# Performance work log

Measured on AMD Instinct MI355X. Metric: run time of the kernel, lower is better.

Reference implementation:

```python
import jax, jax.numpy as jnp
import numpy as np

EPS = 1e-3  # keras LayerNormalization default epsilon

def layer_norm(x, gamma, beta):
    mu = jnp.mean(x, axis=-1, keepdims=True)
    var = jnp.var(x, axis=-1, keepdims=True)
    return (x - mu) * jax.lax.rsqrt(var + EPS) * gamma + beta

def setup_inputs() -> dict:
    key = jax.random.key(0)
    ks = jax.random.split(key, 10)
    B, N, FD, AD, PD, DP = 4, 512, 256, 256, 128, 64
    s = lambda k, *sh: jax.random.normal(k, sh, dtype=jnp.float32)
    return {
        "F": s(ks[0], B, N, FD),
        "D": s(ks[1], B, N, N, DP),
        "Wq": s(ks[2], FD, AD) / np.sqrt(FD),
        "Wk": s(ks[3], FD, AD) / np.sqrt(FD),
        "Wv": s(ks[4], FD, AD) / np.sqrt(FD),
        "g_f": jnp.ones((FD,), jnp.float32),
        "b_f": jnp.zeros((FD,), jnp.float32),
        "g_p": jnp.ones((DP,), jnp.float32),
        "b_p": jnp.zeros((DP,), jnp.float32),
        "W_pt": s(ks[5], DP, PD) / np.sqrt(DP),
        "b_pt": jnp.zeros((PD,), jnp.float32),
        "W_ph": s(ks[6], PD, 1) / np.sqrt(PD),
    }

def reference(F, D, Wq, Wk, Wv, g_f, b_f, g_p, b_p, W_pt, b_pt, W_ph):
    # features path
    Fn = layer_norm(F, g_f, b_f)                       # [B,N,FD]
    Q = Fn @ Wq                                        # [B,N,AD]
    K = Fn @ Wk
    V = Fn @ Wv
    # pair-bias path: LN -> Dense(pairs_dim)+bias -> Dense(num_heads=1)
    Bn = layer_norm(D, g_p, b_p)                       # [B,N,N,DP]
    Bt = Bn @ W_pt + b_pt                              # [B,N,N,PD]
    bias = (Bt @ W_ph)[..., 0]                         # [B,N,N]
    scalar = 1.0 / jnp.sqrt(jnp.float32(Q.shape[-1]))
    A = jnp.einsum('bqd,bkd->bqk', Q, K) + bias        # QK^T + pair bias
    A = jax.nn.softmax(scalar * A, axis=-1)
    O = jnp.einsum('bqk,bkd->bqd', A, V)               # [B,N,AD]
    return jnp.sum(O, axis=-1)                         # [B,N]
```

## Files before the change

kernel.cpp:

```cpp
#include <hip/hip_runtime.h>
#include <cstddef>
#include <cstdint>

#define OFF_GW    0
#define OFF_WV    64
#define OFF_SC    320
#define OFF_VSUM  384
#define OFF_Q     2432
#define OFF_KT    526720
#define OFF_BIAS  1051008

typedef float v4f __attribute__((ext_vector_type(4)));
typedef float v2f __attribute__((ext_vector_type(2)));

__global__ __launch_bounds__(256) void k0_consts(
    const float* __restrict__ Wv, const float* __restrict__ g_p,
    const float* __restrict__ b_p, const float* __restrict__ W_pt,
    const float* __restrict__ b_pt, const float* __restrict__ W_ph,
    float* __restrict__ ws) {
  int t = threadIdx.x;
  if (blockIdx.x < 64) {
    int row = blockIdx.x * 4 + (t >> 6);
    int l = t & 63;
    float s = 0.f;
#pragma unroll
    for (int j = 0; j < 4; ++j) s += Wv[row * 256 + l + 64 * j];
    for (int m = 32; m >= 1; m >>= 1) s += __shfl_xor(s, m);
    if (l == 0) ws[OFF_WV + row] = s;
  } else {
    __shared__ float wc_s[64];
    __shared__ float wph_s[128];
    if (t < 128) wph_s[t] = W_ph[t];
    __syncthreads();
    int c = t >> 2, sub = t & 3;
    float wc = 0.f;
#pragma unroll
    for (int j = 0; j < 32; ++j)
      wc += W_pt[c * 128 + sub * 32 + j] * wph_s[sub * 32 + j];
    wc += __shfl_xor(wc, 1);
    wc += __shfl_xor(wc, 2);
    if (sub == 0) {
      wc_s[c] = wc;
      ws[OFF_GW + c] = g_p[c] * wc;
    }
    __syncthreads();
    if (t == 0) {
      float sg = 0.f, bc = 0.f;
      for (int cc = 0; cc < 64; ++cc) {
        sg += g_p[cc] * wc_s[cc];
        bc += b_p[cc] * wc_s[cc];
      }
      for (int p = 0; p < 128; ++p) bc += b_pt[p] * wph_s[p];
      ws[OFF_SC] = sg;
      ws[OFF_SC + 1] = bc;
    }
  }
}

__global__ __launch_bounds__(256, 4) void kf_proj_bias(
    const float* __restrict__ F, const float* __restrict__ Wq,
    const float* __restrict__ Wk, const float* __restrict__ g_f,
    const float* __restrict__ b_f, const float* __restrict__ D,
    float* __restrict__ ws) {
  __shared__ __align__(16) float fn[8][260];
  __shared__ float smu[8], srn[8];
  __shared__ __align__(16) float gws[64];
  int t = threadIdx.x;

  if (blockIdx.x >= 512) {
    if (t < 64) gws[t] = ws[OFF_GW + t];
    float sum_gw = ws[OFF_SC];
    float bconst = ws[OFF_SC + 1];
    __syncthreads();

    int e = (blockIdx.x - 512) * 256 + t;
    const v4f* ep = (const v4f*)(D + (size_t)e * 64);
    v4f x[16];
#pragma unroll
    for (int p = 0; p < 16; ++p) x[p] = ep[p];
    float s1 = 0.f, s2 = 0.f, sw = 0.f;
#pragma unroll
    for (int p = 0; p < 16; ++p) {
      v4f xx = x[p];
      v4f gv = *(const v4f*)(&gws[p * 4]);
      s1 += xx.x + xx.y + xx.z + xx.w;
      s2 += xx.x * xx.x + xx.y * xx.y + xx.z * xx.z + xx.w * xx.w;
      sw += xx.x * gv.x + xx.y * gv.y + xx.z * gv.z + xx.w * gv.w;
    }
    float mu = s1 * (1.f / 64.f);
    float var = s2 * (1.f / 64.f) - mu * mu;
    float rn = rsqrtf(var + 1e-3f);
    ws[OFF_BIAS + e] = (rn * (sw - mu * sum_gw) + bconst) * 0.0625f;
    return;
  }

  int g = blockIdx.x >> 1, h = blockIdx.x & 1;
  int row0 = g * 8;
  const float* Fp = F + (size_t)row0 * 256;
#pragma unroll
  for (int k = 0; k < 8; ++k) fn[k][t] = Fp[k * 256 + t];
  __syncthreads();
  int r = t >> 5, l32 = t & 31;
  float s1 = 0.f, s2 = 0.f;
#pragma unroll
  for (int m = 0; m < 8; ++m) {
    float x = fn[r][l32 + 32 * m];
    s1 += x;
    s2 += x * x;
  }
  for (int m = 16; m >= 1; m >>= 1) {
    s1 += __shfl_xor(s1, m);
    s2 += __shfl_xor(s2, m);
  }
  if (l32 == 0) {
    float mu = s1 * (1.f / 256.f);
    float var = s2 * (1.f / 256.f) - mu * mu;
    smu[r] = mu;
    srn[r] = rsqrtf(var + 1e-3f);
  }
  __syncthreads();
  float gf = g_f[t], bf = b_f[t];
#pragma unroll
  for (int k = 0; k < 8; ++k)
    fn[k][t] = (fn[k][t] - smu[k]) * srn[k] * gf + bf;
  __syncthreads();
  if (h == 0) {
    const float* wv = ws + OFF_WV;
    float s = 0.f;
#pragma unroll
    for (int m = 0; m < 8; ++m) s += fn[r][l32 + 32 * m] * wv[l32 + 32 * m];
    for (int m = 16; m >= 1; m >>= 1) s += __shfl_xor(s, m);
    if (l32 == 0) ws[OFF_VSUM + row0 + r] = s;
  }
  int matsel = t >> 7;
  int col = h * 128 + (t & 127);
  const float* W = matsel ? Wk : Wq;
  float acc[8] = {0, 0, 0, 0, 0, 0, 0, 0};
#pragma unroll 2
  for (int f = 0; f < 256; f += 4) {
    float w0 = W[(f + 0) * 256 + col];
    float w1 = W[(f + 1) * 256 + col];
    float w2 = W[(f + 2) * 256 + col];
    float w3 = W[(f + 3) * 256 + col];
#pragma unroll
    for (int k = 0; k < 8; ++k) {
      v4f x = *(const v4f*)(&fn[k][f]);
      acc[k] = fmaf(x.w, w3,
               fmaf(x.z, w2, fmaf(x.y, w1, fmaf(x.x, w0, acc[k]))));
    }
  }
  if (matsel == 0) {
    float* Out = ws + OFF_Q + (size_t)row0 * 256 + col;
#pragma unroll
    for (int k = 0; k < 8; ++k) Out[k * 256] = acc[k];
  } else {
    int bb = row0 >> 9, r0b = row0 & 511;
    float* Out = ws + OFF_KT + (size_t)bb * 131072 + (size_t)col * 512 + r0b;
    v4f o0 = {acc[0], acc[1], acc[2], acc[3]};
    v4f o1 = {acc[4], acc[5], acc[6], acc[7]};
    *(v4f*)Out = o0;
    *(v4f*)(Out + 4) = o1;
  }
}

__global__ __launch_bounds__(256) void kb2_attn(
    const float* __restrict__ ws, float* __restrict__ out) {
  __shared__ float Sx[4][512];
  __shared__ __align__(16) float Qs[4][256];
  __shared__ float vs[512];
  int t = threadIdx.x;
  int w = t >> 6, l = t & 63;
  int b = blockIdx.x >> 7, tile = blockIdx.x & 127;
  int rowbase = b * 512 + tile * 4;

#pragma unroll
  for (int k = 0; k < 4; ++k)
    Qs[k][t] = ws[OFF_Q + (size_t)(rowbase + k) * 256 + t];
  vs[t] = ws[OFF_VSUM + b * 512 + t];
  vs[t + 256] = ws[OFF_VSUM + b * 512 + 256 + t];
  const float* bb = ws + OFF_BIAS + (size_t)rowbase * 512;
#pragma unroll
  for (int rr = 0; rr < 4; ++rr) {
    Sx[rr][t] = bb[rr * 512 + t];
    Sx[rr][t + 256] = bb[rr * 512 + 256 + t];
  }
  __syncthreads();

  const float* Ktb = ws + OFF_KT + (size_t)b * 131072;
  float a0[4] = {0, 0, 0, 0}, a1[4] = {0, 0, 0, 0};
#pragma unroll 2
  for (int f4 = 0; f4 < 64; ++f4) {
    v4f qv0 = *(const v4f*)(&Qs[0][f4 * 4]);
    v4f qv1 = *(const v4f*)(&Qs[1][f4 * 4]);
    v4f qv2 = *(const v4f*)(&Qs[2][f4 * 4]);
    v4f qv3 = *(const v4f*)(&Qs[3][f4 * 4]);
#pragma unroll
    for (int ff = 0; ff < 4; ++ff) {
      v2f kv = *(const v2f*)(Ktb + (size_t)(f4 * 4 + ff) * 512 + 2 * t);
      a0[0] += qv0[ff] * kv.x; a1[0] += qv0[ff] * kv.y;
      a0[1] += qv1[ff] * kv.x; a1[1] += qv1[ff] * kv.y;
      a0[2] += qv2[ff] * kv.x; a1[2] += qv2[ff] * kv.y;
      a0[3] += qv3[ff] * kv.x; a1[3] += qv3[ff] * kv.y;
    }
  }
#pragma unroll
  for (int rr = 0; rr < 4; ++rr) {
    Sx[rr][2 * t]     += a0[rr] * 0.0625f;
    Sx[rr][2 * t + 1] += a1[rr] * 0.0625f;
  }
  __syncthreads();

  float m = -1e30f;
#pragma unroll
  for (int j = 0; j < 8; ++j) m = fmaxf(m, Sx[w][l + 64 * j]);
  for (int mm = 32; mm >= 1; mm >>= 1) m = fmaxf(m, __shfl_xor(m, mm));
  float se = 0.f, sv = 0.f;
#pragma unroll
  for (int j = 0; j < 8; ++j) {
    float ev = __expf(Sx[w][l + 64 * j] - m);
    se += ev;
    sv += ev * vs[l + 64 * j];
  }
  for (int mm = 32; mm >= 1; mm >>= 1) {
    se += __shfl_xor(se, mm);
    sv += __shfl_xor(sv, mm);
  }
  if (l == 0) out[rowbase + w] = sv / se;
}

extern "C" void kernel_launch(void* const* d_in, const int* in_sizes, int n_in,
                              void* d_out, int out_size, void* d_ws,
                              size_t ws_size, hipStream_t stream) {
  const float* F    = (const float*)d_in[0];
  const float* D    = (const float*)d_in[1];
  const float* Wq   = (const float*)d_in[2];
  const float* Wk   = (const float*)d_in[3];
  const float* Wv   = (const float*)d_in[4];
  const float* g_f  = (const float*)d_in[5];
  const float* b_f  = (const float*)d_in[6];
  const float* g_p  = (const float*)d_in[7];
  const float* b_p  = (const float*)d_in[8];
  const float* W_pt = (const float*)d_in[9];
  const float* b_pt = (const float*)d_in[10];
  const float* W_ph = (const float*)d_in[11];
  float* out = (float*)d_out;
  float* ws = (float*)d_ws;

  k0_consts<<<65, 256, 0, stream>>>(Wv, g_p, b_p, W_pt, b_pt, W_ph, ws);
  kf_proj_bias<<<4608, 256, 0, stream>>>(F, Wq, Wk, g_f, b_f, D, ws);
  kb2_attn<<<512, 256, 0, stream>>>(ws, out);
}
```

Before: 411.4 us.

## Stage D pair-bias loads through swizzled LDS with coalesced double-buffered reads

The pair-bias branch used to have each thread read one 64-float row of D (256 B strided per lane). It now has each wave load 16 rows at a time with fully coalesced float4 loads into a swizzled LDS staging buffer, double-buffered across four stages. Four lanes then cooperate per row and finish the reduction with shuffles. This targets poor coalescing on the dominant 268 MB D read, at the cost of 32 KB of shared memory per block (hurting occupancy for the projection blocks too) and extra block-wide barriers.

Result: faster. 399.0 us (-3.0%).

```diff
diff --git a/kernel.cpp b/kernel.cpp
--- a/kernel.cpp
+++ b/kernel.cpp
@@ -62,7 +62,7 @@
     const float* __restrict__ Wk, const float* __restrict__ g_f,
     const float* __restrict__ b_f, const float* __restrict__ D,
     float* __restrict__ ws) {
-  __shared__ __align__(16) float fn[8][260];
+  __shared__ __align__(16) float shmem[8192];
   __shared__ float smu[8], srn[8];
   __shared__ __align__(16) float gws[64];
   int t = threadIdx.x;
@@ -71,29 +71,77 @@
     if (t < 64) gws[t] = ws[OFF_GW + t];
     float sum_gw = ws[OFF_SC];
     float bconst = ws[OFF_SC + 1];
-    __syncthreads();
-
-    int e = (blockIdx.x - 512) * 256 + t;
-    const v4f* ep = (const v4f*)(D + (size_t)e * 64);
-    v4f x[16];
-#pragma unroll
-    for (int p = 0; p < 16; ++p) x[p] = ep[p];
-    float s1 = 0.f, s2 = 0.f, sw = 0.f;
-#pragma unroll
-    for (int p = 0; p < 16; ++p) {
-      v4f xx = x[p];
-      v4f gv = *(const v4f*)(&gws[p * 4]);
-      s1 += xx.x + xx.y + xx.z + xx.w;
-      s2 += xx.x * xx.x + xx.y * xx.y + xx.z * xx.z + xx.w * xx.w;
-      sw += xx.x * gv.x + xx.y * gv.y + xx.z * gv.z + xx.w * gv.w;
-    }
-    float mu = s1 * (1.f / 64.f);
-    float var = s2 * (1.f / 64.f) - mu * mu;
-    float rn = rsqrtf(var + 1e-3f);
-    ws[OFF_BIAS + e] = (rn * (sw - mu * sum_gw) + bconst) * 0.0625f;
+    int w = t >> 6, l = t & 63;
+    int el = l & 15, q = l >> 4;
+    size_t e0 = (size_t)(blockIdx.x - 512) * 256;
+    const float* Dbase = D + (e0 + w * 64) * 64;
+    float* stg0 = shmem + (w * 2 + 0) * 1024;
+    float* stg1 = shmem + (w * 2 + 1) * 1024;
+    int wi0 = (l * 4)       ^ (((l >> 4)     & 7) << 2);
+    int wi1 = (l * 4 + 256) ^ (((l >> 4) + 4 & 7) << 2);
+    int wi2 = (l * 4 + 512) ^ (((l >> 4)     & 7) << 2);
+    int wi3 = (l * 4 + 768) ^ (((l >> 4) + 4 & 7) << 2);
+    __syncthreads();
+
+    v4f A0, A1, A2, A3, B0, B1, B2, B3;
+#define KF_LOAD(R0, R1, R2, R3, S)                                          \
+    {                                                                       \
+      const v4f* p = (const v4f*)(Dbase + (S) * 1024);                      \
+      R0 = p[l]; R1 = p[l + 64]; R2 = p[l + 128]; R3 = p[l + 192];          \
+    }
+#define KF_STORE(BUF, R0, R1, R2, R3)                                       \
+    {                                                                       \
+      *(v4f*)((BUF) + wi0) = R0; *(v4f*)((BUF) + wi1) = R1;                 \
+      *(v4f*)((BUF) + wi2) = R2; *(v4f*)((BUF) + wi3) = R3;                 \
+    }
+#define KF_CONSUME(BUF, S)                                                  \
+    {                                                                       \
+      float s1 = 0.f, s2 = 0.f, sw_ = 0.f;                                  \
+      _Pragma("unroll")                                                     \
+      for (int i = 0; i < 4; ++i) {                                         \
+        int idx = (el * 64 + q * 16 + i * 4) ^ ((el & 7) << 2);             \
+        v4f x = *(const v4f*)((BUF) + idx);                                 \
+        v4f gv = *(const v4f*)(&gws[q * 16 + i * 4]);                       \
+        s1 += x.x + x.y + x.z + x.w;                                        \
+        s2 += x.x * x.x + x.y * x.y + x.z * x.z + x.w * x.w;                \
+        sw_ += x.x * gv.x + x.y * gv.y + x.z * gv.z + x.w * gv.w;           \
+      }                                                                     \
+      s1 += __shfl_xor(s1, 16); s2 += __shfl_xor(s2, 16);                   \
+      sw_ += __shfl_xor(sw_, 16);                                           \
+      s1 += __shfl_xor(s1, 32); s2 += __shfl_xor(s2, 32);                   \
+      sw_ += __shfl_xor(sw_, 32);                                           \
+      if (q == 0) {                                                         \
+        float mu = s1 * (1.f / 64.f);                                       \
+        float var = s2 * (1.f / 64.f) - mu * mu;                            \
+        float rn = rsqrtf(var + 1e-3f);                                     \
+        ws[OFF_BIAS + e0 + w * 64 + (S) * 16 + el] =                        \
+            (rn * (sw_ - mu * sum_gw) + bconst) * 0.0625f;                  \
+      }                                                                     \
+    }
+
+    KF_LOAD(A0, A1, A2, A3, 0)
+    KF_STORE(stg0, A0, A1, A2, A3)
+    KF_LOAD(B0, B1, B2, B3, 1)
+    __syncthreads();
+    KF_CONSUME(stg0, 0)
+    KF_STORE(stg1, B0, B1, B2, B3)
+    KF_LOAD(A0, A1, A2, A3, 2)
+    __syncthreads();
+    KF_CONSUME(stg1, 1)
+    KF_STORE(stg0, A0, A1, A2, A3)
+    KF_LOAD(B0, B1, B2, B3, 3)
+    __syncthreads();
+    KF_CONSUME(stg0, 2)
+    KF_STORE(stg1, B0, B1, B2, B3)
+    __syncthreads();
+    KF_CONSUME(stg1, 3)
+#undef KF_LOAD
+#undef KF_STORE
+#undef KF_CONSUME
     return;
   }
 
+  float (*fn)[260] = (float (*)[260])shmem;
   int g = blockIdx.x >> 1, h = blockIdx.x & 1;
   int row0 = g * 8;
   const float* Fp = F + (size_t)row0 * 256;
```
